# Kernel tuning notes

Measured on AMD Instinct MI355X. Metric: run time of the kernel, lower is better.

Reference implementation:

```python
import jax, jax.numpy as jnp
import numpy as np

S = 2048      # sequence length
D = 2048      # d_model
H = 16        # n_heads
E = 128       # d_head


def setup_inputs() -> dict:
    key = jax.random.key(0)
    kx, kw = jax.random.split(key)
    x = jax.random.normal(kx, (S, D), dtype=jnp.float32)
    # xavier_normal for fan_in=D, fan_out=3*E per head
    std = float(np.sqrt(2.0 / (D + 3 * E)))
    w_qkv = jax.random.normal(kw, (H, D, 3 * E), dtype=jnp.float32) * std
    return {"x": x, "w_qkv": w_qkv}


def reference(x, w_qkv):
    # qkv: [h, s, 3e]
    qkv = jnp.einsum('sd,hde->hse', x, w_qkv)
    q, k, v = jnp.split(qkv, 3, axis=-1)            # each [h, s, e]
    scores = jnp.einsum('hse,hte->hst', q, k) / jnp.sqrt(jnp.asarray(E, x.dtype))
    attn = jax.nn.softmax(scores, axis=-1)          # [h, s, t]
    out = jnp.einsum('hst,hte->hse', attn, v)       # [h, s, e]
    # concat heads: [s, h*e]
    return out.transpose(1, 0, 2).reshape(x.shape[0], -1)
```

## Files before the change

### kernel.cpp

```cpp
#include <hip/hip_runtime.h>

#define SEQ 2048
#define DMODEL 2048
#define NHEAD 16
#define EHEAD 128
#define NE3 384

using short8 = __attribute__((ext_vector_type(8))) short;
using f32x4  = __attribute__((ext_vector_type(4))) float;
using f32x16 = __attribute__((ext_vector_type(16))) float;
using uint4v = __attribute__((ext_vector_type(4))) unsigned int;

__device__ __forceinline__ unsigned short f32_to_bf16(float f) {
    unsigned int u = __float_as_uint(f);
    unsigned int rounding = 0x7fffu + ((u >> 16) & 1u);
    u += rounding;
    return (unsigned short)(u >> 16);
}

__device__ __forceinline__ void async_load16(const void* g, void* l) {
    __builtin_amdgcn_global_load_lds(
        (const __attribute__((address_space(1))) unsigned int*)g,
        (__attribute__((address_space(3))) unsigned int*)l, 16, 0, 0);
}

__global__ void cast_x_kernel(const float* __restrict__ x, unsigned short* __restrict__ xb) {
    int i = (blockIdx.x * blockDim.x + threadIdx.x) * 4;
    float4 v = *(const float4*)(x + i);
    ushort4 o = make_ushort4(f32_to_bf16(v.x), f32_to_bf16(v.y), f32_to_bf16(v.z), f32_to_bf16(v.w));
    *(ushort4*)(xb + i) = o;
}

__global__ void transpose_w_kernel(const float* __restrict__ w, unsigned short* __restrict__ wT) {
    __shared__ float tile[64][65];
    int h  = blockIdx.z;
    int d0 = blockIdx.x * 64;
    int n0 = blockIdx.y * 64;
    int t = threadIdx.x;
    int rr = t >> 4;
    int cc = (t & 15) * 4;
#pragma unroll
    for (int i = 0; i < 4; i++) {
        float4 v = *(const float4*)&w[(size_t)(h * DMODEL + d0 + rr + i * 16) * NE3 + n0 + cc];
        tile[rr + i * 16][cc + 0] = v.x;
        tile[rr + i * 16][cc + 1] = v.y;
        tile[rr + i * 16][cc + 2] = v.z;
        tile[rr + i * 16][cc + 3] = v.w;
    }
    __syncthreads();
#pragma unroll
    for (int i = 0; i < 4; i++) {
        int n = rr + i * 16;
        ushort4 o;
        o.x = f32_to_bf16(tile[cc + 0][n]);
        o.y = f32_to_bf16(tile[cc + 1][n]);
        o.z = f32_to_bf16(tile[cc + 2][n]);
        o.w = f32_to_bf16(tile[cc + 3][n]);
        *(ushort4*)&wT[(size_t)(h * NE3 + n0 + n) * DMODEL + d0 + cc] = o;
    }
}

__global__ __launch_bounds__(256, 2) void qkv_gemm128(
        const unsigned short* __restrict__ A,
        const unsigned short* __restrict__ B,
        unsigned short* __restrict__ Q,
        unsigned short* __restrict__ Kb,
        unsigned short* __restrict__ Vt) {
    __shared__ __attribute__((aligned(16))) unsigned short sA[128 * 32];
    __shared__ __attribute__((aligned(16))) unsigned short sB[128 * 32];
    const int mb = blockIdx.x, nb = blockIdx.y;
    const int tid = threadIdx.x;
    const int wave = tid >> 6, lane = tid & 63;
    const int r = lane & 15, q = lane >> 4;
    const int wm = wave & 1, wn = wave >> 1;

    const unsigned short* gA0 = A + (size_t)(mb * 128 + (tid >> 2)) * DMODEL + (tid & 3) * 8;
    const unsigned short* gA1 = gA0 + (size_t)64 * DMODEL;
    const unsigned short* gB0 = B + (size_t)(nb * 128 + (tid >> 2)) * DMODEL + (tid & 3) * 8;
    const unsigned short* gB1 = gB0 + (size_t)64 * DMODEL;
    unsigned short* lA0 = sA + wave * 512;
    unsigned short* lA1 = sA + 2048 + wave * 512;
    unsigned short* lB0 = sB + wave * 512;
    unsigned short* lB1 = sB + 2048 + wave * 512;

    f32x4 acc[4][4] = {};
    for (int k0 = 0; k0 < DMODEL; k0 += 32) {
        __syncthreads();
        async_load16(gA0 + k0, lA0);
        async_load16(gA1 + k0, lA1);
        async_load16(gB0 + k0, lB0);
        async_load16(gB1 + k0, lB1);
        __syncthreads();
        short8 a[4], b[4];
#pragma unroll
        for (int i = 0; i < 4; i++) a[i] = *(const short8*)&sA[(wm * 64 + i * 16 + r) * 32 + q * 8];
#pragma unroll
        for (int j = 0; j < 4; j++) b[j] = *(const short8*)&sB[(wn * 64 + j * 16 + r) * 32 + q * 8];
#pragma unroll
        for (int i = 0; i < 4; i++)
#pragma unroll
            for (int j = 0; j < 4; j++)
                acc[i][j] = __builtin_amdgcn_mfma_f32_16x16x32_bf16(a[i], b[j], acc[i][j], 0, 0, 0);
    }

    const int h = nb / 3, sel = nb % 3;
#pragma unroll
    for (int i = 0; i < 4; i++) {
#pragma unroll
        for (int j = 0; j < 4; j++) {
            const int row0 = mb * 128 + wm * 64 + i * 16 + q * 4;
            const int col  = wn * 64 + j * 16 + r;
            if (sel == 2) {
                ushort4 v;
                v.x = f32_to_bf16(acc[i][j][0]);
                v.y = f32_to_bf16(acc[i][j][1]);
                v.z = f32_to_bf16(acc[i][j][2]);
                v.w = f32_to_bf16(acc[i][j][3]);
                *(ushort4*)&Vt[((size_t)h * EHEAD + col) * SEQ + row0] = v;
            } else {
                unsigned short* dst = (sel == 0) ? Q : Kb;
#pragma unroll
                for (int reg = 0; reg < 4; reg++)
                    dst[((size_t)h * SEQ + row0 + reg) * EHEAD + col] = f32_to_bf16(acc[i][j][reg]);
            }
        }
    }
}

__global__ __launch_bounds__(256, 2) void flash_attn(
        const unsigned short* __restrict__ Qg,
        const unsigned short* __restrict__ Kg,
        const unsigned short* __restrict__ Vtg,
        float* __restrict__ out) {
    extern __shared__ __attribute__((aligned(16))) unsigned short lds[];
    unsigned short* sQ  = lds;
    unsigned short* sK0 = lds + 8192;
    unsigned short* sV0 = lds + 24576;

    const int tid = threadIdx.x;
    const int wave = tid >> 6, lane = tid & 63;
    const int l31 = lane & 31, q2 = lane >> 5;
    const int wm = wave >> 1, wn = wave & 1;
    const int b = blockIdx.x;
    const int h  = (b & 7) + (((b >> 3) >> 5) << 3);
    const int m0 = ((b >> 3) & 31) * 64;

    const unsigned short* Qh  = Qg  + ((size_t)h * SEQ + m0) * EHEAD;
    const unsigned short* Kh0 = Kg  + (size_t)h * SEQ * EHEAD;
    const unsigned short* Vh  = Vtg + (size_t)h * EHEAD * SEQ;

    const int qkRow = lane >> 4;
    const int qkPos = lane & 15;
    const int vRow  = lane >> 3;
    const int vPos  = lane & 7;

    const unsigned short* gK[4];
    const unsigned short* gV[4];
#pragma unroll
    for (int c = 0; c < 4; c++) {
        int u = wave * 4 + c;
        int row = u * 4 + qkRow;
        int ch = qkPos ^ (row & 7);
        gK[c] = Kh0 + (size_t)row * EHEAD + ch * 8;
        int rv = u * 8 + vRow;
        int cv = vPos ^ (rv & 7);
        gV[c] = Vh + (size_t)rv * SEQ + cv * 8;
        async_load16(Qh + (size_t)row * EHEAD + ch * 8, sQ + u * 512);
        async_load16(gK[c], sK0 + u * 512);
        async_load16(gV[c], sV0 + u * 512);
        gK[c] += 64 * EHEAD;
        gV[c] += 64;
    }
    __syncthreads();

    short8 bq[8];
    {
        const int row = wm * 32 + l31;
#pragma unroll
        for (int kc = 0; kc < 8; kc++) {
            int p = (kc * 2 + q2) ^ (row & 7);
            bq[kc] = *(const short8*)&sQ[row * 128 + p * 8];
        }
    }

    const unsigned short* kp[8];
    const unsigned short* vp[8];
    const int rowA = wn * 32 + l31;
#pragma unroll
    for (int kc = 0; kc < 8; kc++)
        kp[kc] = sK0 + rowA * 128 + (((kc * 2 + q2) ^ (rowA & 7)) * 8);
#pragma unroll
    for (int et = 0; et < 4; et++)
#pragma unroll
        for (int kc2 = 0; kc2 < 2; kc2++) {
            int rowV = et * 32 + l31;
            int cch = wn * 4 + kc2 * 2 + q2;
            vp[et * 2 + kc2] = sV0 + rowV * 64 + ((cch ^ (rowV & 7)) * 8);
        }

    const float c1 = 0.12752405856f;
    f32x16 acc_o[4] = {};
    float l_acc = 0.f;

    auto body = [&](const int cur, const int nxt, bool pref) {
        if (pref) {
#pragma unroll
            for (int c = 0; c < 4; c++) {
                async_load16(gK[c], sK0 + nxt + (wave * 4 + c) * 512);
                gK[c] += 64 * EHEAD;
            }
#pragma unroll
            for (int c = 0; c < 4; c++) {
                async_load16(gV[c], sV0 + nxt + (wave * 4 + c) * 512);
                gV[c] += 64;
            }
        }

        f32x16 st = {};
#pragma unroll
        for (int kc = 0; kc < 8; kc++) {
            short8 ak = *(const short8*)(kp[kc] + cur);
            st = __builtin_amdgcn_mfma_f32_32x32x16_bf16(ak, bq[kc], st, 0, 0, 0);
        }

        unsigned int pk[8];
#pragma unroll
        for (int t = 0; t < 8; t++) {
            float p0 = __builtin_amdgcn_exp2f(st[2 * t] * c1);
            float p1 = __builtin_amdgcn_exp2f(st[2 * t + 1] * c1);
            l_acc += p0 + p1;
            unsigned int u0 = __float_as_uint(p0) + 0x8000u;
            unsigned int u1 = __float_as_uint(p1) + 0x8000u;
            pk[t] = __builtin_amdgcn_perm(u1, u0, 0x07060302u);
        }

        short8 fr[2];
#pragma unroll
        for (int kc2 = 0; kc2 < 2; kc2++) {
            unsigned int a0 = pk[kc2 * 4 + 0], a1 = pk[kc2 * 4 + 1];
            unsigned int a2 = pk[kc2 * 4 + 2], a3 = pk[kc2 * 4 + 3];
            unsigned int s0 = (unsigned int)__shfl_xor((int)a0, 32);
            unsigned int s1 = (unsigned int)__shfl_xor((int)a1, 32);
            unsigned int s2 = (unsigned int)__shfl_xor((int)a2, 32);
            unsigned int s3 = (unsigned int)__shfl_xor((int)a3, 32);
            uint4v t;
            t.x = q2 ? s2 : a0;
            t.y = q2 ? s3 : a1;
            t.z = q2 ? a2 : s0;
            t.w = q2 ? a3 : s1;
            fr[kc2] = __builtin_bit_cast(short8, t);
        }

#pragma unroll
        for (int et = 0; et < 4; et++)
#pragma unroll
            for (int kc2 = 0; kc2 < 2; kc2++) {
                short8 bv = *(const short8*)(vp[et * 2 + kc2] + cur);
                acc_o[et] = __builtin_amdgcn_mfma_f32_32x32x16_bf16(fr[kc2], bv, acc_o[et], 0, 0, 0);
            }
        __syncthreads();
    };

    for (int ip = 0; ip < SEQ / 128; ip++) {
        body(0, 8192, true);
        body(8192, 0, ip != SEQ / 128 - 1);
    }

    l_acc += __shfl_xor(l_acc, 32);

    float* fl = (float*)lds;
#pragma unroll
    for (int et = 0; et < 4; et++) {
        if ((et >> 1) != wn) {
#pragma unroll
            for (int rg = 0; rg < 4; rg++) {
                f32x4 v;
                v[0] = acc_o[et][rg * 4 + 0];
                v[1] = acc_o[et][rg * 4 + 1];
                v[2] = acc_o[et][rg * 4 + 2];
                v[3] = acc_o[et][rg * 4 + 3];
                *(f32x4*)&fl[(size_t)(((wm * 4 + et) * 4 + rg) * 256) + lane * 4] = v;
            }
        }
    }
    fl[8192 + (wm * 2 + wn) * 32 + l31] = l_acc;
    __syncthreads();

    float invq[4][4];
#pragma unroll
    for (int rg = 0; rg < 4; rg++)
#pragma unroll
        for (int i = 0; i < 4; i++) {
            int qy = i + 4 * q2 + 8 * rg;
            float lt = fl[8192 + (wm * 2 + 0) * 32 + qy] + fl[8192 + (wm * 2 + 1) * 32 + qy];
            invq[rg][i] = 1.0f / lt;
        }

#pragma unroll
    for (int et = 0; et < 4; et++) {
        if ((et >> 1) == wn) {
#pragma unroll
            for (int rg = 0; rg < 4; rg++) {
                f32x4 v = *(const f32x4*)&fl[(size_t)(((wm * 4 + et) * 4 + rg) * 256) + lane * 4];
#pragma unroll
                for (int i = 0; i < 4; i++) {
                    int mrow = i + 4 * q2 + 8 * rg;
                    out[(size_t)(m0 + wm * 32 + mrow) * DMODEL + h * EHEAD + et * 32 + l31] =
                        (acc_o[et][rg * 4 + i] + v[i]) * invq[rg][i];
                }
            }
        }
    }
}

extern "C" void kernel_launch(void* const* d_in, const int* in_sizes, int n_in,
                              void* d_out, int out_size, void* d_ws, size_t ws_size,
                              hipStream_t stream) {
    const float* x = (const float*)d_in[0];
    const float* w = (const float*)d_in[1];
    float* out = (float*)d_out;

    char* ws = (char*)d_ws;
    unsigned short* xb = (unsigned short*)(ws);
    unsigned short* wT = (unsigned short*)(ws + 8388608);
    unsigned short* Q  = (unsigned short*)(ws + 33554432);
    unsigned short* Kb = (unsigned short*)(ws + 41943040);
    unsigned short* Vt = (unsigned short*)(ws + 50331648);

    static bool attr_set = false;
    if (!attr_set) {
        hipFuncSetAttribute((const void*)flash_attn,
                            hipFuncAttributeMaxDynamicSharedMemorySize, 81920);
        attr_set = true;
    }

    cast_x_kernel<<<SEQ * DMODEL / (256 * 4), 256, 0, stream>>>(x, xb);
    transpose_w_kernel<<<dim3(DMODEL / 64, NE3 / 64, NHEAD), 256, 0, stream>>>(w, wT);
    qkv_gemm128<<<dim3(SEQ / 128, (NHEAD * NE3) / 128), 256, 0, stream>>>(xb, wT, Q, Kb, Vt);
    flash_attn<<<512, 256, 81920, stream>>>(Q, Kb, Vt, out);
}
```

Measured before the change: 204.7 us.

## Rewrite QKV GEMM as 256x256 tile with 4-stage async LDS pipeline

```diff
diff --git a/kernel.cpp b/kernel.cpp
--- a/kernel.cpp
+++ b/kernel.cpp
@@ -23,6 +23,13 @@
         (const __attribute__((address_space(1))) unsigned int*)g,
         (__attribute__((address_space(3))) unsigned int*)l, 16, 0, 0);
 }
+
+#define WG_BARRIER()                              \
+    do {                                          \
+        asm volatile("" ::: "memory");            \
+        __builtin_amdgcn_s_barrier();             \
+        asm volatile("" ::: "memory");            \
+    } while (0)
 
 __global__ void cast_x_kernel(const float* __restrict__ x, unsigned short* __restrict__ xb) {
     int i = (blockIdx.x * blockDim.x + threadIdx.x) * 4;
@@ -60,68 +67,134 @@
     }
 }
 
-__global__ __launch_bounds__(256, 2) void qkv_gemm128(
+template <int B, bool STAGE, int VM>
+__device__ __forceinline__ void qkv_kstep(
+        unsigned short* lds, f32x4 (&acc)[8][4],
+        const unsigned short*& sA0, const unsigned short*& sA1,
+        const unsigned short*& sB0, const unsigned short*& sB1,
+        const int wave, const int aoff, const int boff) {
+    constexpr int B3 = (B + 3) & 3;
+    const unsigned short* LA = lds + B * 16384 + aoff;
+    const unsigned short* LB = lds + B * 16384 + boff;
+
+    short8 a0[4], bb[4];
+#pragma unroll
+    for (int mf = 0; mf < 4; ++mf) a0[mf] = *(const short8*)(LA + mf * 512);
+#pragma unroll
+    for (int nf = 0; nf < 4; ++nf) bb[nf] = *(const short8*)(LB + nf * 512);
+    if constexpr (STAGE) {
+        async_load16(sA0, lds + B3 * 16384 + wave * 512);
+        async_load16(sA1, lds + B3 * 16384 + 4096 + wave * 512);
+    }
+    sA0 += 32; sA1 += 32;
+    WG_BARRIER();
+    __builtin_amdgcn_s_setprio(1);
+#pragma unroll
+    for (int mf = 0; mf < 4; ++mf)
+#pragma unroll
+        for (int nf = 0; nf < 4; ++nf)
+            acc[mf][nf] = __builtin_amdgcn_mfma_f32_16x16x32_bf16(a0[mf], bb[nf], acc[mf][nf], 0, 0, 0);
+    __builtin_amdgcn_s_setprio(0);
+    WG_BARRIER();
+
+    short8 a1[4];
+#pragma unroll
+    for (int mf = 0; mf < 4; ++mf) a1[mf] = *(const short8*)(LA + (4 + mf) * 512);
+    if constexpr (STAGE) {
+        async_load16(sB0, lds + B3 * 16384 + 8192 + wave * 512);
+        async_load16(sB1, lds + B3 * 16384 + 12288 + wave * 512);
+    }
+    sB0 += 32; sB1 += 32;
+    if constexpr (VM == 8)      asm volatile("s_waitcnt vmcnt(8)" ::: "memory");
+    else if constexpr (VM == 4) asm volatile("s_waitcnt vmcnt(4)" ::: "memory");
+    else if constexpr (VM == 0) asm volatile("s_waitcnt vmcnt(0)" ::: "memory");
+    WG_BARRIER();
+    __builtin_amdgcn_s_setprio(1);
+#pragma unroll
+    for (int mf = 0; mf < 4; ++mf)
+#pragma unroll
+        for (int nf = 0; nf < 4; ++nf)
+            acc[4 + mf][nf] = __builtin_amdgcn_mfma_f32_16x16x32_bf16(a1[mf], bb[nf], acc[4 + mf][nf], 0, 0, 0);
+    __builtin_amdgcn_s_setprio(0);
+    WG_BARRIER();
+}
+
+__global__ __launch_bounds__(512, 2) void qkv_gemm256(
         const unsigned short* __restrict__ A,
-        const unsigned short* __restrict__ B,
+        const unsigned short* __restrict__ Bm,
         unsigned short* __restrict__ Q,
         unsigned short* __restrict__ Kb,
         unsigned short* __restrict__ Vt) {
-    __shared__ __attribute__((aligned(16))) unsigned short sA[128 * 32];
-    __shared__ __attribute__((aligned(16))) unsigned short sB[128 * 32];
+    extern __shared__ __attribute__((aligned(16))) unsigned short lds[];
     const int mb = blockIdx.x, nb = blockIdx.y;
     const int tid = threadIdx.x;
     const int wave = tid >> 6, lane = tid & 63;
     const int r = lane & 15, q = lane >> 4;
-    const int wm = wave & 1, wn = wave >> 1;
-
-    const unsigned short* gA0 = A + (size_t)(mb * 128 + (tid >> 2)) * DMODEL + (tid & 3) * 8;
-    const unsigned short* gA1 = gA0 + (size_t)64 * DMODEL;
-    const unsigned short* gB0 = B + (size_t)(nb * 128 + (tid >> 2)) * DMODEL + (tid & 3) * 8;
-    const unsigned short* gB1 = gB0 + (size_t)64 * DMODEL;
-    unsigned short* lA0 = sA + wave * 512;
-    unsigned short* lA1 = sA + 2048 + wave * 512;
-    unsigned short* lB0 = sB + wave * 512;
-    unsigned short* lB1 = sB + 2048 + wave * 512;
-
-    f32x4 acc[4][4] = {};
-    for (int k0 = 0; k0 < DMODEL; k0 += 32) {
-        __syncthreads();
-        async_load16(gA0 + k0, lA0);
-        async_load16(gA1 + k0, lA1);
-        async_load16(gB0 + k0, lB0);
-        async_load16(gB1 + k0, lB1);
-        __syncthreads();
-        short8 a[4], b[4];
-#pragma unroll
-        for (int i = 0; i < 4; i++) a[i] = *(const short8*)&sA[(wm * 64 + i * 16 + r) * 32 + q * 8];
-#pragma unroll
-        for (int j = 0; j < 4; j++) b[j] = *(const short8*)&sB[(wn * 64 + j * 16 + r) * 32 + q * 8];
-#pragma unroll
-        for (int i = 0; i < 4; i++)
-#pragma unroll
-            for (int j = 0; j < 4; j++)
-                acc[i][j] = __builtin_amdgcn_mfma_f32_16x16x32_bf16(a[i], b[j], acc[i][j], 0, 0, 0);
-    }
-
-    const int h = nb / 3, sel = nb % 3;
-#pragma unroll
-    for (int i = 0; i < 4; i++) {
-#pragma unroll
-        for (int j = 0; j < 4; j++) {
-            const int row0 = mb * 128 + wm * 64 + i * 16 + q * 4;
-            const int col  = wn * 64 + j * 16 + r;
+    const int wm = wave >> 2, wn = wave & 3;
+
+    const int c0 = tid, c1 = tid + 512;
+    const int rr0 = (c0 >> 2) & 15, rr1 = (c1 >> 2) & 15;
+    const int r0 = ((c0 >> 6) << 4) + rr0, k0c = ((c0 & 3) ^ (rr0 & 3)) << 3;
+    const int r1 = ((c1 >> 6) << 4) + rr1, k1c = ((c1 & 3) ^ (rr1 & 3)) << 3;
+
+    const unsigned short* sA0 = A  + (size_t)(mb * 256 + r0) * DMODEL + k0c;
+    const unsigned short* sA1 = A  + (size_t)(mb * 256 + r1) * DMODEL + k1c;
+    const unsigned short* sB0 = Bm + (size_t)(nb * 256 + r0) * DMODEL + k0c;
+    const unsigned short* sB1 = Bm + (size_t)(nb * 256 + r1) * DMODEL + k1c;
+
+#pragma unroll
+    for (int t = 0; t < 3; ++t) {
+        async_load16(sA0 + t * 32, lds + t * 16384 + wave * 512);
+        async_load16(sA1 + t * 32, lds + t * 16384 + 4096 + wave * 512);
+        async_load16(sB0 + t * 32, lds + t * 16384 + 8192 + wave * 512);
+        async_load16(sB1 + t * 32, lds + t * 16384 + 12288 + wave * 512);
+    }
+    sA0 += 96; sA1 += 96; sB0 += 96; sB1 += 96;
+
+    const int qs = q ^ (r & 3);
+    const int aoff = wm * 4096 + r * 32 + qs * 8;
+    const int boff = 8192 + wn * 2048 + r * 32 + qs * 8;
+
+    f32x4 acc[8][4] = {};
+    asm volatile("s_waitcnt vmcnt(8)" ::: "memory");
+    WG_BARRIER();
+
+    for (int i = 0; i < 15; ++i) {
+        qkv_kstep<0, true, 8>(lds, acc, sA0, sA1, sB0, sB1, wave, aoff, boff);
+        qkv_kstep<1, true, 8>(lds, acc, sA0, sA1, sB0, sB1, wave, aoff, boff);
+        qkv_kstep<2, true, 8>(lds, acc, sA0, sA1, sB0, sB1, wave, aoff, boff);
+        qkv_kstep<3, true, 8>(lds, acc, sA0, sA1, sB0, sB1, wave, aoff, boff);
+    }
+    qkv_kstep<0, true,  8>(lds, acc, sA0, sA1, sB0, sB1, wave, aoff, boff);
+    qkv_kstep<1, false, 4>(lds, acc, sA0, sA1, sB0, sB1, wave, aoff, boff);
+    qkv_kstep<2, false, 0>(lds, acc, sA0, sA1, sB0, sB1, wave, aoff, boff);
+    qkv_kstep<3, false, -1>(lds, acc, sA0, sA1, sB0, sB1, wave, aoff, boff);
+
+    const int mbase = mb * 256 + wm * 128;
+    const int nbase = nb * 256 + wn * 64;
+#pragma unroll
+    for (int nf = 0; nf < 4; ++nf) {
+        const int cb = nbase + nf * 16;
+        const int head = cb / 384;
+        const int rem = cb - head * 384;
+        const int sel = rem >> 7;
+        const int e = (rem & 127) + r;
+#pragma unroll
+        for (int mf = 0; mf < 8; ++mf) {
+            const int row0 = mbase + mf * 16 + q * 4;
+            const f32x4 v = acc[mf][nf];
             if (sel == 2) {
-                ushort4 v;
-                v.x = f32_to_bf16(acc[i][j][0]);
-                v.y = f32_to_bf16(acc[i][j][1]);
-                v.z = f32_to_bf16(acc[i][j][2]);
-                v.w = f32_to_bf16(acc[i][j][3]);
-                *(ushort4*)&Vt[((size_t)h * EHEAD + col) * SEQ + row0] = v;
+                ushort4 o;
+                o.x = f32_to_bf16(v[0]);
+                o.y = f32_to_bf16(v[1]);
+                o.z = f32_to_bf16(v[2]);
+                o.w = f32_to_bf16(v[3]);
+                *(ushort4*)&Vt[((size_t)head * EHEAD + e) * SEQ + row0] = o;
             } else {
-                unsigned short* dst = (sel == 0) ? Q : Kb;
-#pragma unroll
-                for (int reg = 0; reg < 4; reg++)
-                    dst[((size_t)h * SEQ + row0 + reg) * EHEAD + col] = f32_to_bf16(acc[i][j][reg]);
+                unsigned short* dst = sel ? Kb : Q;
+#pragma unroll
+                for (int reg = 0; reg < 4; ++reg)
+                    dst[((size_t)head * SEQ + row0 + reg) * EHEAD + e] = f32_to_bf16(v[reg]);
             }
         }
     }
@@ -331,11 +404,13 @@
     if (!attr_set) {
         hipFuncSetAttribute((const void*)flash_attn,
                             hipFuncAttributeMaxDynamicSharedMemorySize, 81920);
+        hipFuncSetAttribute((const void*)qkv_gemm256,
+                            hipFuncAttributeMaxDynamicSharedMemorySize, 131072);
         attr_set = true;
     }
 
     cast_x_kernel<<<SEQ * DMODEL / (256 * 4), 256, 0, stream>>>(x, xb);
     transpose_w_kernel<<<dim3(DMODEL / 64, NE3 / 64, NHEAD), 256, 0, stream>>>(w, wT);
-    qkv_gemm128<<<dim3(SEQ / 128, (NHEAD * NE3) / 128), 256, 0, stream>>>(xb, wT, Q, Kb, Vt);
+    qkv_gemm256<<<dim3(SEQ / 256, (NHEAD * NE3) / 256), 512, 131072, stream>>>(xb, wT, Q, Kb, Vt);
     flash_attn<<<512, 256, 81920, stream>>>(Q, Kb, Vt, out);
 }
```

After: 209.2 us. 2.2% more time.
